# Performance work log

Hardware: AMD Instinct MI355X
Metric: run time of the kernel (lower is better)

## Reference

```python
import jax, jax.numpy as jnp
import numpy as np

N_NODES = 100000
N_EDGES = 3200000
IN_F = 500
HID = 64
OUT_F = 64
ALPHA = 0.1
K = 10


def setup_inputs() -> dict:
    key = jax.random.key(0)
    ks = jax.random.split(key, 8)
    x = jax.random.normal(ks[0], (N_NODES, IN_F), dtype=jnp.float32)
    edge_src = jax.random.randint(ks[1], (N_EDGES,), 0, N_NODES, dtype=jnp.int32)
    edge_dst = jax.random.randint(ks[2], (N_EDGES,), 0, N_NODES, dtype=jnp.int32)
    edge_weight = jax.random.uniform(ks[3], (N_EDGES,), dtype=jnp.float32)
    W1 = jax.random.normal(ks[4], (IN_F, HID), dtype=jnp.float32) * (1.0 / np.sqrt(IN_F))
    b1 = jnp.zeros((HID,), dtype=jnp.float32)
    W2 = jax.random.normal(ks[5], (HID, OUT_F), dtype=jnp.float32) * (1.0 / np.sqrt(HID))
    b2 = jnp.zeros((OUT_F,), dtype=jnp.float32)
    return {"x": x, "edge_src": edge_src, "edge_dst": edge_dst,
            "edge_weight": edge_weight, "W1": W1, "b1": b1, "W2": W2, "b2": b2}


def _spmm(edge_src, edge_dst, edge_weight, z):
    # sparse adj @ z : gather rows at src, scale by edge weight, scatter-add at dst
    msg = edge_weight[:, None] * z[edge_src]          # [E, C]
    return jax.ops.segment_sum(msg, edge_dst, num_segments=N_NODES)


def reference(x, edge_src, edge_dst, edge_weight, W1, b1, W2, b2):
    # MLP encoder (dropout is identity at inference)
    h = jax.nn.relu(x @ W1 + b1) @ W2 + b2            # [N, OUT_F]
    # APPNP propagation: z_{k+1} = (1-alpha) * A z_k + alpha * h
    z = h
    for _ in range(K):
        z = (1.0 - ALPHA) * _spmm(edge_src, edge_dst, edge_weight, z) + ALPHA * h
    return z
```

## Files before the change

### kernel.cpp

```cpp
#include <hip/hip_runtime.h>

#define N_NODES 100000
#define N_EDGES 3200000
#define IN_F 500
#define HID 64
#define OUT_F 64
#define ALPHA 0.1f
#define K_ITERS 10
#define SCAN_B ((N_NODES + 255) / 256)

#define NPART 8
#define PART_N (N_NODES / NPART)
#define SUB_N 1563
#define NBUCK 64
#define FILL_GRID 2048

#define SPLIT_CHUNK 2560
#define SPLIT_ROUNDS 10
#define SPLIT_GRID (N_EDGES / SPLIT_CHUNK)

#define KPAD 512

typedef unsigned short ushort_t;
typedef unsigned int uint_t;
typedef __attribute__((ext_vector_type(8))) short bf16x8;
typedef __attribute__((ext_vector_type(4))) float f32x4;
typedef int iv2 __attribute__((ext_vector_type(2)));

__device__ __forceinline__ float bf2f(ushort_t v) {
    union { uint_t u; float f; } c; c.u = ((uint_t)v) << 16; return c.f;
}
__device__ __forceinline__ ushort_t f2b(float f) {
    union { float f; uint_t u; } c; c.f = f;
    uint_t u = c.u + 0x7fffu + ((c.u >> 16) & 1u);
    return (ushort_t)(u >> 16);
}
__device__ __forceinline__ float bflo(uint_t u) {
    union { uint_t u; float f; } c; c.u = u << 16; return c.f;
}
__device__ __forceinline__ float bfhi(uint_t u) {
    union { uint_t u; float f; } c; c.u = u & 0xffff0000u; return c.f;
}
__device__ __forceinline__ uint_t packbf(float a, float b) {
    return (uint_t)f2b(a) | ((uint_t)f2b(b) << 16);
}
__device__ __forceinline__ bf16x8 pack8(float4 a, float4 b) {
    bf16x8 r;
    r[0] = (short)f2b(a.x); r[1] = (short)f2b(a.y);
    r[2] = (short)f2b(a.z); r[3] = (short)f2b(a.w);
    r[4] = (short)f2b(b.x); r[5] = (short)f2b(b.y);
    r[6] = (short)f2b(b.z); r[7] = (short)f2b(b.w);
    return r;
}

__global__ __launch_bounds__(256) void prep_weights(
    const float* __restrict__ W1, const float* __restrict__ W2,
    ushort_t* __restrict__ w1t, ushort_t* __restrict__ w2t)
{
    int i = blockIdx.x * 256 + threadIdx.x;
    if (i < 64 * KPAD) {
        int c = i >> 9, k = i & (KPAD - 1);
        float v = (k < IN_F) ? W1[k * HID + c] : 0.f;
        w1t[c * KPAD + k] = f2b(v);
    } else {
        int j = i - 64 * KPAD;
        if (j < 64 * 64) {
            int c = j >> 6, k = j & 63;
            w2t[c * 64 + k] = f2b(W2[k * OUT_F + c]);
        }
    }
}

__global__ __launch_bounds__(256, 2) void mlp_mfma(
    const float* __restrict__ x, const ushort_t* __restrict__ w1t,
    const float* __restrict__ b1, const ushort_t* __restrict__ w2t,
    const float* __restrict__ b2, ushort_t* __restrict__ hb,
    ushort_t* __restrict__ ahb)
{
    __shared__ float xs[2][64][32];
    __shared__ ushort_t hs[4][16][64];

    const int tid  = threadIdx.x;
    const int lane = tid & 63;
    const int wid  = tid >> 6;
    const int r16  = lane & 15;
    const int kg   = lane >> 4;
    const int block_row = blockIdx.x * 64;
    const int rowbase   = block_row + wid * 16;

    const int s_row0 = tid >> 3;
    const int s_row1 = s_row0 + 32;
    const int s_c    = tid & 7;
    int grow0 = block_row + s_row0; if (grow0 > N_NODES - 1) grow0 = N_NODES - 1;
    int grow1 = block_row + s_row1; if (grow1 > N_NODES - 1) grow1 = N_NODES - 1;
    const float* gx0 = x + (size_t)grow0 * IN_F + s_c * 4;
    const float* gx1 = x + (size_t)grow1 * IN_F + s_c * 4;
    char* xsb = (char*)&xs[0][0][0];
    const int ld0 = s_row0 * 128 + ((s_c ^ (s_row0 & 7)) * 16);
    const int ld1 = s_row1 * 128 + ((s_c ^ (s_row1 & 7)) * 16);

    f32x4 acc[4];
    #pragma unroll
    for (int t = 0; t < 4; ++t) acc[t] = (f32x4){0.f, 0.f, 0.f, 0.f};

    const int lrow  = wid * 16 + r16;
    const int swz   = lrow & 7;
    const int rbase = lrow * 128;
    const int off_a = rbase + (((kg * 2)     ^ swz) * 16);
    const int off_b = rbase + (((kg * 2 + 1) ^ swz) * 16);

#define XMM(PA, PB, KS) do {                                      \
        bf16x8 af_ = pack8(PA, PB);                               \
        _Pragma("unroll")                                         \
        for (int t = 0; t < 4; ++t) {                             \
            bf16x8 bw_ = *(const bf16x8*)&w1t[(t * 16 + r16) * KPAD + (KS) * 32 + kg * 8]; \
            acc[t] = __builtin_amdgcn_mfma_f32_16x16x32_bf16(af_, bw_, acc[t], 0, 0, 0);   \
        }                                                         \
    } while (0)

    float4 va = *(const float4*)(gx0);
    float4 vb = *(const float4*)(gx1);
    *(float4*)(xsb + ld0) = va;
    *(float4*)(xsb + ld1) = vb;
    __syncthreads();

    int cur = 0;
    for (int ks = 0; ks < 15; ++ks) {
        if (ks < 14) {
            va = *(const float4*)(gx0 + (ks + 1) * 32);
            vb = *(const float4*)(gx1 + (ks + 1) * 32);
        }
        const char* bb = xsb + cur * 8192;
        float4 fa = *(const float4*)(bb + off_a);
        float4 fb = *(const float4*)(bb + off_b);
        XMM(fa, fb, ks);
        __syncthreads();
        if (ks < 14) {
            char* wb = xsb + (cur ^ 1) * 8192;
            *(float4*)(wb + ld0) = va;
            *(float4*)(wb + ld1) = vb;
        }
        __syncthreads();
        cur ^= 1;
    }

    {
        const float4 z4 = make_float4(0.f, 0.f, 0.f, 0.f);
        int arow = rowbase + r16;
        int lrow2 = (arow < N_NODES) ? arow : (N_NODES - 1);
        const float* xr = x + (size_t)lrow2 * IN_F;
        float4 ta = (kg <= 2) ? *(const float4*)(xr + 480 + kg * 8) : z4;
        float4 tb = (kg <= 1) ? *(const float4*)(xr + 484 + kg * 8) : z4;
        XMM(ta, tb, 15);
    }
#undef XMM

    #pragma unroll
    for (int t = 0; t < 4; ++t) {
        float bb = b1[t * 16 + r16];
        #pragma unroll
        for (int r = 0; r < 4; ++r) {
            float h = fmaxf(acc[t][r] + bb, 0.f);
            int row = kg * 4 + r;
            int col = (t * 16 + r16) ^ ((row & 7) << 3);
            hs[wid][row][col] = f2b(h);
        }
    }
    __syncthreads();

    f32x4 acc2[4];
    #pragma unroll
    for (int t = 0; t < 4; ++t) acc2[t] = (f32x4){0.f, 0.f, 0.f, 0.f};

    #pragma unroll
    for (int ks = 0; ks < 2; ++ks) {
        int colr = (ks * 32 + kg * 8) ^ ((r16 & 7) << 3);
        bf16x8 ha = *(const bf16x8*)&hs[wid][r16][colr];
        #pragma unroll
        for (int t = 0; t < 4; ++t) {
            bf16x8 wb = *(const bf16x8*)&w2t[(t * 16 + r16) * 64 + ks * 32 + kg * 8];
            acc2[t] = __builtin_amdgcn_mfma_f32_16x16x32_bf16(ha, wb, acc2[t], 0, 0, 0);
        }
    }

    #pragma unroll
    for (int t = 0; t < 4; ++t) {
        float bb = b2[t * 16 + r16];
        #pragma unroll
        for (int r = 0; r < 4; ++r) {
            int orow = rowbase + kg * 4 + r;
            if (orow < N_NODES) {
                float v = acc2[t][r] + bb;
                hb[orow * 64 + t * 16 + r16]  = f2b(v);
                ahb[orow * 64 + t * 16 + r16] = f2b(ALPHA * v);
            }
        }
    }
}

__global__ __launch_bounds__(256) void zero_cnt(int* __restrict__ cnt)
{
    int i = blockIdx.x * 256 + threadIdx.x;
    if (i < N_NODES) cnt[i] = 0;
}

__global__ __launch_bounds__(256) void count_keys(
    const int* __restrict__ key, int* __restrict__ cnt)
{
    int i = blockIdx.x * 256 + threadIdx.x;
    if (i < N_EDGES) atomicAdd(&cnt[key[i]], 1);
}

__global__ __launch_bounds__(256) void scan_block_sums(
    const int* __restrict__ cnt, int* __restrict__ bsum)
{
    int i = blockIdx.x * 256 + threadIdx.x;
    int v = (i < N_NODES) ? cnt[i] : 0;
    for (int off = 32; off; off >>= 1) v += __shfl_down(v, off);
    __shared__ int ws_[4];
    if ((threadIdx.x & 63) == 0) ws_[threadIdx.x >> 6] = v;
    __syncthreads();
    if (threadIdx.x == 0) bsum[blockIdx.x] = ws_[0] + ws_[1] + ws_[2] + ws_[3];
}

__global__ __launch_bounds__(512) void scan_partials(
    const int* __restrict__ bsum, int* __restrict__ boff)
{
    int t = threadIdx.x;
    int v = (t < SCAN_B) ? bsum[t] : 0;
    int lane = t & 63, w = t >> 6;
    int x = v;
    for (int off = 1; off < 64; off <<= 1) {
        int y = __shfl_up(x, off);
        if (lane >= off) x += y;
    }
    __shared__ int wsum[8];
    if (lane == 63) wsum[w] = x;
    __syncthreads();
    if (w == 0) {
        int s = (lane < 8) ? wsum[lane] : 0;
        for (int off = 1; off < 8; off <<= 1) {
            int y = __shfl_up(s, off);
            if (lane >= off) s += y;
        }
        if (lane < 8) wsum[lane] = s;
    }
    __syncthreads();
    int wpre = (w == 0) ? 0 : wsum[w - 1];
    if (t < SCAN_B) boff[t] = wpre + x - v;
}

__global__ __launch_bounds__(256) void scan_final(
    const int* __restrict__ cnt, const int* __restrict__ boff,
    int* __restrict__ row_start, int* __restrict__ pos,
    int* __restrict__ pcur)
{
    int i = blockIdx.x * 256 + threadIdx.x;
    int v = (i < N_NODES) ? cnt[i] : 0;
    int lane = threadIdx.x & 63, w = threadIdx.x >> 6;
    int x = v;
    for (int off = 1; off < 64; off <<= 1) {
        int y = __shfl_up(x, off);
        if (lane >= off) x += y;
    }
    __shared__ int wsum[4];
    if (lane == 63) wsum[w] = x;
    __syncthreads();
    int wpre = 0;
    for (int ww = 0; ww < w; ++ww) wpre += wsum[ww];
    int excl = wpre + x - v;
    int r = boff[blockIdx.x] + excl;
    if (i < N_NODES) {
        row_start[i] = r; pos[i] = r;
        int rel = i % PART_N;
        if (rel % SUB_N == 0) {
            pcur[(i / PART_N) * 8 + rel / SUB_N] = r;
        }
    }
    if (i == 0) row_start[N_NODES] = N_EDGES;
}

__global__ __launch_bounds__(256) void split_edges(
    const int* __restrict__ esrc, const int* __restrict__ edst,
    const float* __restrict__ ew, int* __restrict__ pcur,
    int2* __restrict__ sbuf)
{
    __shared__ int lhist[NBUCK];
    __shared__ int lbase[NBUCK];
    const int tid  = threadIdx.x;
    const int base = blockIdx.x * SPLIT_CHUNK;

    if (tid < NBUCK) lhist[tid] = 0;
    __syncthreads();

    int bk[SPLIT_ROUNDS];
    int dl[SPLIT_ROUNDS];
    #pragma unroll
    for (int k = 0; k < SPLIT_ROUNDS; ++k) {
        int d = edst[base + k * 256 + tid];
        int p = d / PART_N;
        int rel = d - p * PART_N;
        bk[k] = p * 8 + rel / SUB_N;
        dl[k] = rel;
        atomicAdd(&lhist[bk[k]], 1);
    }
    __syncthreads();
    if (tid < NBUCK) lbase[tid] = atomicAdd(&pcur[tid], lhist[tid]);
    __syncthreads();

    #pragma unroll
    for (int k = 0; k < SPLIT_ROUNDS; ++k) {
        int slot = atomicAdd(&lbase[bk[k]], 1);
        int i = base + k * 256 + tid;
        sbuf[slot] = make_int2((dl[k] << 17) | esrc[i],
                               __float_as_int(0.9f * ew[i]));
    }
}

__global__ __launch_bounds__(256) void fill_b(
    const int2* __restrict__ sbuf, const int* __restrict__ row_start,
    int* __restrict__ pos, int2* __restrict__ csr)
{
    const int b   = blockIdx.x & (NBUCK - 1);
    const int p   = b >> 3, sub = b & 7;
    const int dlo = p * PART_N + sub * SUB_N;
    int dhi = dlo + SUB_N;
    const int pend = p * PART_N + PART_N;
    if (dhi > pend) dhi = pend;
    const int lo_e = row_start[dlo];
    const int hi_e = row_start[dhi];
    const int stride = (FILL_GRID / NBUCK) * 256;
    for (int i = lo_e + (blockIdx.x >> 6) * 256 + (int)threadIdx.x; i < hi_e;
         i += stride) {
        iv2 e = __builtin_nontemporal_load((const iv2*)sbuf + i);
        int d = p * PART_N + (((unsigned)e.x) >> 17);
        int q = atomicAdd(&pos[d], 1);
        csr[q] = make_int2(e.x & 0x1ffff, e.y);
    }
}

__global__ __launch_bounds__(256) void sort_rows(
    const int* __restrict__ row_start, int2* __restrict__ csr)
{
    const int node = blockIdx.x * 4 + (threadIdx.x >> 6);
    const int lane = threadIdx.x & 63;
    const int s0 = row_start[node];
    const int s1 = row_start[node + 1];
    int n = s1 - s0; if (n > 64) n = 64;
    int key = 0x7fffffff;
    int val = 0;
    if (lane < n) { int2 e = csr[s0 + lane]; key = e.x; val = e.y; }
    #pragma unroll
    for (int k = 2; k <= 64; k <<= 1) {
        #pragma unroll
        for (int j = k >> 1; j > 0; j >>= 1) {
            int pk = __shfl_xor(key, j, 64);
            int pv = __shfl_xor(val, j, 64);
            bool lower   = (lane & j) == 0;
            bool asc     = (lane & k) == 0;
            bool takeMin = (lower == asc);
            bool pick    = takeMin ? (pk < key) : (pk > key);
            if (pick) { key = pk; val = pv; }
        }
    }
    if (lane < n) csr[s0 + lane] = make_int2(key, val);
}

template <bool FINAL>
__global__ __launch_bounds__(256) void spmm_kernel(
    const int* __restrict__ row_start, const int2* __restrict__ csr,
    const ushort_t* __restrict__ zin, const ushort_t* __restrict__ ahb,
    void* __restrict__ zout)
{
    const int node = blockIdx.x * 4 + (threadIdx.x >> 6);
    const int lane = threadIdx.x & 63;
    const int g = lane >> 3;
    const int q = lane & 7;
    const int s0 = __builtin_amdgcn_readfirstlane(row_start[node]);
    const int s1 = __builtin_amdgcn_readfirstlane(row_start[node + 1]);

    float a0=0.f,a1=0.f,a2=0.f,a3=0.f,a4=0.f,a5=0.f,a6=0.f,a7=0.f;
    if (g == 0) {
        uint4 t = *(const uint4*)&ahb[node * 64 + 8 * q];
        a0 = bflo(t.x); a1 = bfhi(t.x); a2 = bflo(t.y); a3 = bfhi(t.y);
        a4 = bflo(t.z); a5 = bfhi(t.z); a6 = bflo(t.w); a7 = bfhi(t.w);
    }

#define FMA8(WV, ZV) do { \
        a0 = fmaf((WV), bflo((ZV).x), a0); a1 = fmaf((WV), bfhi((ZV).x), a1); \
        a2 = fmaf((WV), bflo((ZV).y), a2); a3 = fmaf((WV), bfhi((ZV).y), a3); \
        a4 = fmaf((WV), bflo((ZV).z), a4); a5 = fmaf((WV), bfhi((ZV).z), a5); \
        a6 = fmaf((WV), bflo((ZV).w), a6); a7 = fmaf((WV), bfhi((ZV).w), a7); \
    } while (0)

    int j = s0;
    for (; j + 32 <= s1; j += 32) {
        int2 e0 = csr[j + g];
        int2 e1 = csr[j + 8 + g];
        int2 e2 = csr[j + 16 + g];
        int2 e3 = csr[j + 24 + g];
        uint4 z0 = *(const uint4*)&zin[e0.x * 64 + 8 * q];
        uint4 z1 = *(const uint4*)&zin[e1.x * 64 + 8 * q];
        uint4 z2 = *(const uint4*)&zin[e2.x * 64 + 8 * q];
        uint4 z3 = *(const uint4*)&zin[e3.x * 64 + 8 * q];
        float w0 = __int_as_float(e0.y);
        float w1 = __int_as_float(e1.y);
        float w2 = __int_as_float(e2.y);
        float w3 = __int_as_float(e3.y);
        FMA8(w0, z0);
        FMA8(w1, z1);
        FMA8(w2, z2);
        FMA8(w3, z3);
    }
    for (; j < s1; j += 8) {
        int2 e = make_int2(0, 0);
        int jj = j + g;
        if (jj < s1) e = csr[jj];
        uint4 zt = *(const uint4*)&zin[e.x * 64 + 8 * q];
        float wt = __int_as_float(e.y);
        FMA8(wt, zt);
    }
#undef FMA8

    #pragma unroll
    for (int m = 8; m <= 32; m <<= 1) {
        a0 += __shfl_xor(a0, m, 64); a1 += __shfl_xor(a1, m, 64);
        a2 += __shfl_xor(a2, m, 64); a3 += __shfl_xor(a3, m, 64);
        a4 += __shfl_xor(a4, m, 64); a5 += __shfl_xor(a5, m, 64);
        a6 += __shfl_xor(a6, m, 64); a7 += __shfl_xor(a7, m, 64);
    }

    if (g == 0) {
        if (FINAL) {
            float* op = (float*)zout + node * 64 + 8 * q;
            *(float4*)op       = make_float4(a0, a1, a2, a3);
            *(float4*)(op + 4) = make_float4(a4, a5, a6, a7);
        } else {
            uint4 pk;
            pk.x = packbf(a0, a1); pk.y = packbf(a2, a3);
            pk.z = packbf(a4, a5); pk.w = packbf(a6, a7);
            *(uint4*)&((ushort_t*)zout)[node * 64 + 8 * q] = pk;
        }
    }
}

extern "C" void kernel_launch(void* const* d_in, const int* in_sizes, int n_in,
                              void* d_out, int out_size, void* d_ws, size_t ws_size,
                              hipStream_t stream)
{
    const float* x    = (const float*)d_in[0];
    const int*   esrc = (const int*)d_in[1];
    const int*   edst = (const int*)d_in[2];
    const float* ew   = (const float*)d_in[3];
    const float* W1   = (const float*)d_in[4];
    const float* b1   = (const float*)d_in[5];
    const float* W2   = (const float*)d_in[6];
    const float* b2   = (const float*)d_in[7];
    float* out = (float*)d_out;

    char* p = (char*)d_ws;
    ushort_t* ahb = (ushort_t*)p;  p += (size_t)N_NODES * 64 * 2;
    ushort_t* hb  = (ushort_t*)p;  p += (size_t)N_NODES * 64 * 2;
    ushort_t* zB  = (ushort_t*)p;  p += (size_t)N_NODES * 64 * 2;
    int2*  csr     = (int2*)p;     p += (size_t)N_EDGES * 8;
    int* cnt       = (int*)p;      p += (size_t)N_NODES * 4;
    int* pos       = (int*)p;      p += (size_t)N_NODES * 4;
    int* row_start = (int*)p;      p += (size_t)(N_NODES + 1) * 4;
    int* bsum      = (int*)p;      p += (size_t)SCAN_B * 4;
    int* boff      = (int*)p;      p += (size_t)SCAN_B * 4;
    int* pcur      = (int*)p;      p += (size_t)NBUCK * 4;
    ushort_t* w1t  = (ushort_t*)p; p += (size_t)64 * KPAD * 2;
    ushort_t* w2t  = (ushort_t*)p; p += (size_t)64 * 64 * 2;
    int2* sbuf = (int2*)ahb;

    const int EB = (N_EDGES + 255) / 256;

    hipLaunchKernelGGL(prep_weights, dim3((64 * KPAD + 64 * 64 + 255) / 256),
                       dim3(256), 0, stream, W1, W2, w1t, w2t);

    hipLaunchKernelGGL(zero_cnt, dim3(SCAN_B), dim3(256), 0, stream, cnt);
    hipLaunchKernelGGL(count_keys, dim3(EB), dim3(256), 0, stream, edst, cnt);
    hipLaunchKernelGGL(scan_block_sums, dim3(SCAN_B), dim3(256), 0, stream, cnt, bsum);
    hipLaunchKernelGGL(scan_partials, dim3(1), dim3(512), 0, stream, bsum, boff);
    hipLaunchKernelGGL(scan_final, dim3(SCAN_B), dim3(256), 0, stream,
                       cnt, boff, row_start, pos, pcur);
    hipLaunchKernelGGL(split_edges, dim3(SPLIT_GRID), dim3(256), 0, stream,
                       esrc, edst, ew, pcur, sbuf);
    hipLaunchKernelGGL(fill_b, dim3(FILL_GRID), dim3(256), 0, stream,
                       sbuf, row_start, pos, csr);
    hipLaunchKernelGGL(sort_rows, dim3(N_NODES / 4), dim3(256), 0, stream,
                       row_start, csr);

    hipLaunchKernelGGL(mlp_mfma, dim3((N_NODES + 63) / 64), dim3(256), 0, stream,
                       x, w1t, b1, w2t, b2, hb, ahb);

    const ushort_t* zi = hb;
    for (int it = 0; it < K_ITERS - 1; ++it) {
        ushort_t* zo = (it % 2 == 0) ? zB : hb;
        hipLaunchKernelGGL((spmm_kernel<false>), dim3(N_NODES / 4), dim3(256), 0, stream,
                           row_start, csr, zi, ahb, (void*)zo);
        zi = zo;
    }
    hipLaunchKernelGGL((spmm_kernel<true>), dim3(N_NODES / 4), dim3(256), 0, stream,
                       row_start, csr, zi, ahb, (void*)out);
}
```

Measured before the change: 1.274 ms.

## Replace global per-node atomic counting with bucket histogram and LDS node counts

Per-node edge counting no longer uses 3.2M global atomics over scattered destinations. A coarse 64-bucket histogram is built with shared-memory atomics and scanned to get bucket bases, and edges are split into buckets first. Per-node counts are then computed from the bucketed buffer with LDS atomics, one sub-bucket per block. This adds two small kernels and an extra pass over the split buffer, and reorders the CSR-build pipeline.

```diff
diff --git a/kernel.cpp b/kernel.cpp
--- a/kernel.cpp
+++ b/kernel.cpp
@@ -18,6 +18,12 @@
 #define SPLIT_CHUNK 2560
 #define SPLIT_ROUNDS 10
 #define SPLIT_GRID (N_EDGES / SPLIT_CHUNK)
+
+#define BC_CHUNK 5120
+#define BC_ROUNDS 20
+#define BC_GRID (N_EDGES / BC_CHUNK)
+
+#define NC_PER 8
 
 #define KPAD 512
 
@@ -198,17 +204,48 @@
     }
 }
 
-__global__ __launch_bounds__(256) void zero_cnt(int* __restrict__ cnt)
+__global__ __launch_bounds__(256) void zero_cnt(
+    int* __restrict__ cnt, int* __restrict__ bcnt)
 {
     int i = blockIdx.x * 256 + threadIdx.x;
     if (i < N_NODES) cnt[i] = 0;
-}
-
-__global__ __launch_bounds__(256) void count_keys(
-    const int* __restrict__ key, int* __restrict__ cnt)
-{
-    int i = blockIdx.x * 256 + threadIdx.x;
-    if (i < N_EDGES) atomicAdd(&cnt[key[i]], 1);
+    if (i < NBUCK) bcnt[i] = 0;
+}
+
+__global__ __launch_bounds__(256) void bucket_count(
+    const int* __restrict__ edst, int* __restrict__ bcnt)
+{
+    __shared__ int lh[NBUCK];
+    const int tid = threadIdx.x;
+    if (tid < NBUCK) lh[tid] = 0;
+    __syncthreads();
+    const int base = blockIdx.x * BC_CHUNK;
+    #pragma unroll 4
+    for (int k = 0; k < BC_ROUNDS; ++k) {
+        int d = edst[base + k * 256 + tid];
+        int p = d / PART_N;
+        int rel = d - p * PART_N;
+        atomicAdd(&lh[p * 8 + rel / SUB_N], 1);
+    }
+    __syncthreads();
+    if (tid < NBUCK && lh[tid]) atomicAdd(&bcnt[tid], lh[tid]);
+}
+
+__global__ __launch_bounds__(64) void bucket_scan(
+    const int* __restrict__ bcnt, int* __restrict__ bbase,
+    int* __restrict__ bpcur)
+{
+    int lane = threadIdx.x;
+    int v = bcnt[lane];
+    int x = v;
+    for (int off = 1; off < 64; off <<= 1) {
+        int y = __shfl_up(x, off);
+        if (lane >= off) x += y;
+    }
+    int excl = x - v;
+    bbase[lane] = excl;
+    bpcur[lane] = excl;
+    if (lane == 63) bbase[64] = x;
 }
 
 __global__ __launch_bounds__(256) void scan_block_sums(
@@ -252,8 +289,7 @@
 
 __global__ __launch_bounds__(256) void scan_final(
     const int* __restrict__ cnt, const int* __restrict__ boff,
-    int* __restrict__ row_start, int* __restrict__ pos,
-    int* __restrict__ pcur)
+    int* __restrict__ row_start, int* __restrict__ pos)
 {
     int i = blockIdx.x * 256 + threadIdx.x;
     int v = (i < N_NODES) ? cnt[i] : 0;
@@ -270,19 +306,13 @@
     for (int ww = 0; ww < w; ++ww) wpre += wsum[ww];
     int excl = wpre + x - v;
     int r = boff[blockIdx.x] + excl;
-    if (i < N_NODES) {
-        row_start[i] = r; pos[i] = r;
-        int rel = i % PART_N;
-        if (rel % SUB_N == 0) {
-            pcur[(i / PART_N) * 8 + rel / SUB_N] = r;
-        }
-    }
+    if (i < N_NODES) { row_start[i] = r; pos[i] = r; }
     if (i == 0) row_start[N_NODES] = N_EDGES;
 }
 
 __global__ __launch_bounds__(256) void split_edges(
     const int* __restrict__ esrc, const int* __restrict__ edst,
-    const float* __restrict__ ew, int* __restrict__ pcur,
+    const float* __restrict__ ew, int* __restrict__ bpcur,
     int2* __restrict__ sbuf)
 {
     __shared__ int lhist[NBUCK];
@@ -305,7 +335,7 @@
         atomicAdd(&lhist[bk[k]], 1);
     }
     __syncthreads();
-    if (tid < NBUCK) lbase[tid] = atomicAdd(&pcur[tid], lhist[tid]);
+    if (tid < NBUCK) lbase[tid] = atomicAdd(&bpcur[tid], lhist[tid]);
     __syncthreads();
 
     #pragma unroll
@@ -317,18 +347,43 @@
     }
 }
 
+__global__ __launch_bounds__(256) void node_count(
+    const int2* __restrict__ sbuf, const int* __restrict__ bbase,
+    int* __restrict__ cnt)
+{
+    __shared__ int lh[SUB_N];
+    const int tid = threadIdx.x;
+    const int b   = blockIdx.x & (NBUCK - 1);
+    const int j   = blockIdx.x >> 6;
+    const int p   = b >> 3, sub = b & 7;
+    const int rel0 = sub * SUB_N;
+
+    for (int s = tid; s < SUB_N; s += 256) lh[s] = 0;
+    __syncthreads();
+
+    const int lo = bbase[b];
+    const int hi = bbase[b + 1];
+    for (int i = lo + j * 256 + tid; i < hi; i += NC_PER * 256) {
+        iv2 e = __builtin_nontemporal_load((const iv2*)sbuf + i);
+        int rel = ((unsigned)e.x) >> 17;
+        atomicAdd(&lh[rel - rel0], 1);
+    }
+    __syncthreads();
+
+    for (int s = tid; s < SUB_N; s += 256) {
+        int c = lh[s];
+        if (c) atomicAdd(&cnt[p * PART_N + rel0 + s], c);
+    }
+}
+
 __global__ __launch_bounds__(256) void fill_b(
-    const int2* __restrict__ sbuf, const int* __restrict__ row_start,
+    const int2* __restrict__ sbuf, const int* __restrict__ bbase,
     int* __restrict__ pos, int2* __restrict__ csr)
 {
     const int b   = blockIdx.x & (NBUCK - 1);
-    const int p   = b >> 3, sub = b & 7;
-    const int dlo = p * PART_N + sub * SUB_N;
-    int dhi = dlo + SUB_N;
-    const int pend = p * PART_N + PART_N;
-    if (dhi > pend) dhi = pend;
-    const int lo_e = row_start[dlo];
-    const int hi_e = row_start[dhi];
+    const int p   = b >> 3;
+    const int lo_e = bbase[b];
+    const int hi_e = bbase[b + 1];
     const int stride = (FILL_GRID / NBUCK) * 256;
     for (int i = lo_e + (blockIdx.x >> 6) * 256 + (int)threadIdx.x; i < hi_e;
          i += stride) {
@@ -468,26 +523,31 @@
     int* row_start = (int*)p;      p += (size_t)(N_NODES + 1) * 4;
     int* bsum      = (int*)p;      p += (size_t)SCAN_B * 4;
     int* boff      = (int*)p;      p += (size_t)SCAN_B * 4;
-    int* pcur      = (int*)p;      p += (size_t)NBUCK * 4;
+    int* bcnt      = (int*)p;      p += (size_t)NBUCK * 4;
+    int* bbase     = (int*)p;      p += (size_t)(NBUCK + 1) * 4;
+    int* bpcur     = (int*)p;      p += (size_t)NBUCK * 4;
     ushort_t* w1t  = (ushort_t*)p; p += (size_t)64 * KPAD * 2;
     ushort_t* w2t  = (ushort_t*)p; p += (size_t)64 * 64 * 2;
     int2* sbuf = (int2*)ahb;
 
-    const int EB = (N_EDGES + 255) / 256;
-
     hipLaunchKernelGGL(prep_weights, dim3((64 * KPAD + 64 * 64 + 255) / 256),
                        dim3(256), 0, stream, W1, W2, w1t, w2t);
 
-    hipLaunchKernelGGL(zero_cnt, dim3(SCAN_B), dim3(256), 0, stream, cnt);
-    hipLaunchKernelGGL(count_keys, dim3(EB), dim3(256), 0, stream, edst, cnt);
+    hipLaunchKernelGGL(zero_cnt, dim3(SCAN_B), dim3(256), 0, stream, cnt, bcnt);
+    hipLaunchKernelGGL(bucket_count, dim3(BC_GRID), dim3(256), 0, stream,
+                       edst, bcnt);
+    hipLaunchKernelGGL(bucket_scan, dim3(1), dim3(64), 0, stream,
+                       bcnt, bbase, bpcur);
+    hipLaunchKernelGGL(split_edges, dim3(SPLIT_GRID), dim3(256), 0, stream,
+                       esrc, edst, ew, bpcur, sbuf);
+    hipLaunchKernelGGL(node_count, dim3(NBUCK * NC_PER), dim3(256), 0, stream,
+                       sbuf, bbase, cnt);
     hipLaunchKernelGGL(scan_block_sums, dim3(SCAN_B), dim3(256), 0, stream, cnt, bsum);
     hipLaunchKernelGGL(scan_partials, dim3(1), dim3(512), 0, stream, bsum, boff);
     hipLaunchKernelGGL(scan_final, dim3(SCAN_B), dim3(256), 0, stream,
-                       cnt, boff, row_start, pos, pcur);
-    hipLaunchKernelGGL(split_edges, dim3(SPLIT_GRID), dim3(256), 0, stream,
-                       esrc, edst, ew, pcur, sbuf);
+                       cnt, boff, row_start, pos);
     hipLaunchKernelGGL(fill_b, dim3(FILL_GRID), dim3(256), 0, stream,
-                       sbuf, row_start, pos, csr);
+                       sbuf, bbase, pos, csr);
     hipLaunchKernelGGL(sort_rows, dim3(N_NODES / 4), dim3(256), 0, stream,
                        row_start, csr);
 
```

After: 1.170 ms. 1.09x faster.
